# Performance work log

Hardware: AMD Instinct MI355X
Metric: run time of the kernel (lower is better)

## Reference

```python
import jax, jax.numpy as jnp
import numpy as np

MAX_DEG = 10
COUNTS = [10000, 250000, 300000, 250000, 120000, 40000, 15000, 8000, 4000, 2000, 1000]
STARTS = [int(s) for s in np.cumsum([0] + COUNTS[:-1])]
N_ATOMS = sum(COUNTS)  # 1,000,000
BATCH = 32768
N_TASKS, N_CLASSES = 12, 2
N_FEAT = 75
GC = [64, 64]
DENSE = 128
FD = 256
EPS = 1e-3  # keras BatchNormalization default epsilon


def _bn(x, gamma, beta, mean, var):
    # inference-mode batch norm (moving stats)
    return (x - mean) * jax.lax.rsqrt(var + EPS) * gamma + beta


def _graph_conv(atoms, deg_adjs, W, b):
    # W: [2*MAX_DEG+1, Cin, Cout]; order: (rel_d, self_d) for d=1..10, then self_0
    outs = [atoms[STARTS[0]:STARTS[0] + COUNTS[0]] @ W[2 * MAX_DEG] + b[2 * MAX_DEG]]
    for d in range(1, MAX_DEG + 1):
        rel = jnp.sum(atoms[deg_adjs[d - 1]], axis=1)          # [cnt_d, Cin]
        self_a = atoms[STARTS[d]:STARTS[d] + COUNTS[d]]        # [cnt_d, Cin]
        outs.append(rel @ W[2 * (d - 1)] + b[2 * (d - 1)] + self_a @ W[2 * d - 1] + b[2 * d - 1])
    return jax.nn.relu(jnp.concatenate(outs, axis=0))


def _graph_pool(atoms, deg_adjs):
    outs = [atoms[STARTS[0]:STARTS[0] + COUNTS[0]]]
    for d in range(1, MAX_DEG + 1):
        self_a = atoms[STARTS[d]:STARTS[d] + COUNTS[d]][:, None, :]  # [cnt_d,1,C]
        gathered = atoms[deg_adjs[d - 1]]                            # [cnt_d,d,C]
        outs.append(jnp.max(jnp.concatenate([self_a, gathered], axis=1), axis=1))
    return jnp.concatenate(outs, axis=0)


def setup_inputs() -> dict:
    key = jax.random.key(0)
    ks = jax.random.split(key, 48)
    inp = {}
    inp['atom_features'] = jax.random.normal(ks[0], (N_ATOMS, N_FEAT), jnp.float32)
    inp['degree_slice'] = jnp.asarray(np.stack([np.array(STARTS), np.array(COUNTS)], 1), jnp.int32)
    inp['membership'] = jax.random.randint(ks[1], (N_ATOMS,), 0, BATCH)
    inp['n_samples'] = BATCH
    for d in range(1, MAX_DEG + 1):
        inp[f'deg_adj_{d}'] = jax.random.randint(ks[1 + d], (COUNTS[d], d), 0, N_ATOMS)
    # GraphConv params: stacked [21, Cin, Cout]
    cin = N_FEAT
    for i, cout in enumerate(GC):
        inp[f'gc{i}_W'] = jax.random.normal(ks[12 + 2 * i], (2 * MAX_DEG + 1, cin, cout), jnp.float32) * 0.05
        inp[f'gc{i}_b'] = jnp.zeros((2 * MAX_DEG + 1, cout), jnp.float32)
        cin = cout
    # BatchNorm params (2 after graph convs: C=64; 1 after dense: C=128)
    for j, c in enumerate([GC[0], GC[1], DENSE]):
        inp[f'bn{j}_gamma'] = jnp.ones((c,), jnp.float32)
        inp[f'bn{j}_beta'] = jnp.zeros((c,), jnp.float32)
        inp[f'bn{j}_mean'] = jax.random.normal(ks[20 + j], (c,), jnp.float32) * 0.05
        inp[f'bn{j}_var'] = jax.random.uniform(ks[24 + j], (c,), jnp.float32, 0.5, 1.5)
    inp['dense_W'] = jax.random.normal(ks[30], (GC[-1], DENSE), jnp.float32) * 0.1
    inp['dense_b'] = jnp.zeros((DENSE,), jnp.float32)
    inp['fd0_W'] = jax.random.normal(ks[31], (2 * DENSE, FD), jnp.float32) * 0.06
    inp['fd0_b'] = jnp.zeros((FD,), jnp.float32)
    inp['rd_W'] = jax.random.normal(ks[32], (FD, N_TASKS * N_CLASSES), jnp.float32) * 0.06
    inp['rd_b'] = jnp.zeros((N_TASKS * N_CLASSES,), jnp.float32)
    return inp


def reference(atom_features, degree_slice, membership, n_samples,
              deg_adj_1, deg_adj_2, deg_adj_3, deg_adj_4, deg_adj_5,
              deg_adj_6, deg_adj_7, deg_adj_8, deg_adj_9, deg_adj_10,
              gc0_W, gc0_b, gc1_W, gc1_b,
              bn0_gamma, bn0_beta, bn0_mean, bn0_var,
              bn1_gamma, bn1_beta, bn1_mean, bn1_var,
              bn2_gamma, bn2_beta, bn2_mean, bn2_var,
              dense_W, dense_b, fd0_W, fd0_b, rd_W, rd_b):
    deg_adjs = [deg_adj_1, deg_adj_2, deg_adj_3, deg_adj_4, deg_adj_5,
                deg_adj_6, deg_adj_7, deg_adj_8, deg_adj_9, deg_adj_10]
    gc_W = [gc0_W, gc1_W]
    gc_b = [gc0_b, gc1_b]
    bns = [(bn0_gamma, bn0_beta, bn0_mean, bn0_var),
           (bn1_gamma, bn1_beta, bn1_mean, bn1_var)]
    x = atom_features
    for i in range(2):
        x = _graph_conv(x, deg_adjs, gc_W[i], gc_b[i])
        x = _bn(x, *bns[i])
        x = _graph_pool(x, deg_adjs)
    x = jax.nn.relu(x @ dense_W + dense_b)
    x = _bn(x, bn2_gamma, bn2_beta, bn2_mean, bn2_var)
    # GraphGather: per-molecule sum and max readout, then tanh
    s = jax.ops.segment_sum(x, membership, num_segments=BATCH)
    m = jax.ops.segment_max(x, membership, num_segments=BATCH)
    nf = jnp.tanh(jnp.concatenate([s, m], axis=1))  # [BATCH, 2*DENSE]
    h = jax.nn.relu(nf @ fd0_W + fd0_b)
    logits = (h @ rd_W + rd_b).reshape(BATCH, N_TASKS, N_CLASSES)
    logits = logits[:n_samples]  # TrimGraphOutput (static here)
    output = jax.nn.softmax(logits, axis=-1)
    return output, logits, nf
```

## Files before the change

### kernel.cpp

```cpp
#include <hip/hip_runtime.h>
#include <hip/hip_fp16.h>
#include <math.h>

namespace {

constexpr int NATOMS = 1000000;
constexpr int NBATCH = 32768;
constexpr int kCounts[11] = {10000,250000,300000,250000,120000,40000,15000,8000,4000,2000,1000};
constexpr int kStarts[11] = {0,10000,260000,560000,810000,930000,970000,985000,993000,997000,999000};
constexpr int X16S = 80;

struct AdjPtrs { const int* p[10]; };

typedef _Float16 h2 __attribute__((ext_vector_type(2)));
typedef _Float16 h8 __attribute__((ext_vector_type(8)));
typedef float    f4 __attribute__((ext_vector_type(4)));
union U32H2 { unsigned u; h2 h; };

__device__ __forceinline__ unsigned enc_f32(float x) {
    unsigned u = __float_as_uint(x);
    return (u & 0x80000000u) ? ~u : (u | 0x80000000u);
}
__device__ __forceinline__ float dec_f32(unsigned u) {
    return (u & 0x80000000u) ? __uint_as_float(u & 0x7FFFFFFFu) : __uint_as_float(~u);
}

__device__ __forceinline__ int swzS64d(int row, int k) { return row ^ (((k >> 2) & 7) << 2); }

__global__ __launch_bounds__(256) void cvt_kernel(const float* __restrict__ x,
                                                  __half* __restrict__ x16)
{
    const int row = blockIdx.x * 16 + (threadIdx.x >> 4);
    const int l16 = threadIdx.x & 15;
    if (row >= NATOMS) return;
    const float* __restrict__ xr = x + (size_t)row * 75;
    __half* __restrict__ xo = x16 + (size_t)row * X16S;
    #pragma unroll
    for (int q = 0; q < 5; ++q) {
        const int c = l16 + 16 * q;
        xo[c] = __float2half((c < 75) ? xr[c] : 0.f);
    }
}

__global__ __launch_bounds__(256) void packB_kernel(const float* __restrict__ W,
                                                    uint4* __restrict__ bp,
                                                    int CI, int GH, int KS)
{
    const int total = 11 * 4 * KS * 64;
    const int idx = blockIdx.x * 256 + threadIdx.x;
    if (idx >= total) return;
    const int lane = idx & 63;
    int q = idx >> 6;
    const int ks = q % KS; q /= KS;
    const int ni = q & 3;
    const int deg = q >> 2;
    const int col = ni * 16 + (lane & 15);
    __half vals[8];
    #pragma unroll
    for (int j = 0; j < 8; ++j) {
        const int k = ks * 32 + (lane >> 4) * 8 + j;
        float v = 0.f;
        if (k < GH * 8) {
            if (k < CI) {
                const int m = (deg == 0) ? 20 : (2 * deg - 1);
                v = W[((size_t)m * CI + k) * 64 + col];
            }
        } else {
            const int kk = k - GH * 8;
            if (deg > 0 && kk < CI)
                v = W[((size_t)(2 * (deg - 1)) * CI + kk) * 64 + col];
        }
        vals[j] = __float2half(v);
    }
    bp[idx] = *reinterpret_cast<const uint4*>(vals);
}

__global__ __launch_bounds__(256) void packBd_kernel(const float* __restrict__ Wd,
                                                     uint4* __restrict__ bpd)
{
    const int idx = blockIdx.x * 256 + threadIdx.x;
    if (idx >= 8 * 2 * 64) return;
    const int lane = idx & 63;
    const int q = idx >> 6;
    const int ks = q & 1, ni = q >> 1;
    const int col = ni * 16 + (lane & 15);
    __half vals[8];
    #pragma unroll
    for (int j = 0; j < 8; ++j) {
        const int k = ks * 32 + (lane >> 4) * 8 + j;
        vals[j] = __float2half(Wd[(size_t)k * 128 + col]);
    }
    bpd[idx] = *reinterpret_cast<const uint4*>(vals);
}

template<int D, int STRH, int GH>
__device__ __forceinline__ void stage_rel64_m(const __half* __restrict__ xin,
                                              const int* __restrict__ ad,
                                              int j0, int row, int l8,
                                              __half* __restrict__ s_a)
{
    int idxs[D];
    #pragma unroll
    for (int n = 0; n < D; ++n) idxs[n] = ad[(size_t)(j0 + row) * D + n];
    float2 r[4];
    #pragma unroll
    for (int q = 0; q < 4; ++q) r[q] = make_float2(0.f, 0.f);
    for (int n = 0; n < D; ++n) {
        const uint4 f4v = *reinterpret_cast<const uint4*>(xin + (size_t)idxs[n] * 64 + l8 * 8);
        const __half2* hh = reinterpret_cast<const __half2*>(&f4v);
        #pragma unroll
        for (int q = 0; q < 4; ++q) {
            const float2 v = __half22float2(hh[q]);
            r[q].x += v.x; r[q].y += v.y;
        }
    }
    uint4 o;
    unsigned* ou = reinterpret_cast<unsigned*>(&o);
    #pragma unroll
    for (int q = 0; q < 4; ++q) {
        U32H2 u; u.h = h2{(_Float16)r[q].x, (_Float16)r[q].y};
        ou[q] = u.u;
    }
    *reinterpret_cast<uint4*>(&s_a[row * STRH + (GH + l8) * 8]) = o;
}

template<int STRH, int GH>
__device__ __forceinline__ void stage_rel64_rt_m(const __half* __restrict__ xin,
                                                 const int* __restrict__ ad, int d,
                                                 int j0, int row, int l8,
                                                 __half* __restrict__ s_a)
{
    int idxs[10];
    for (int n = 0; n < d; ++n) idxs[n] = ad[(size_t)(j0 + row) * d + n];
    float2 r[4];
    #pragma unroll
    for (int q = 0; q < 4; ++q) r[q] = make_float2(0.f, 0.f);
    for (int n = 0; n < d; ++n) {
        const uint4 f4v = *reinterpret_cast<const uint4*>(xin + (size_t)idxs[n] * 64 + l8 * 8);
        const __half2* hh = reinterpret_cast<const __half2*>(&f4v);
        #pragma unroll
        for (int q = 0; q < 4; ++q) {
            const float2 v = __half22float2(hh[q]);
            r[q].x += v.x; r[q].y += v.y;
        }
    }
    uint4 o;
    unsigned* ou = reinterpret_cast<unsigned*>(&o);
    #pragma unroll
    for (int q = 0; q < 4; ++q) {
        U32H2 u; u.h = h2{(_Float16)r[q].x, (_Float16)r[q].y};
        ou[q] = u.u;
    }
    *reinterpret_cast<uint4*>(&s_a[row * STRH + (GH + l8) * 8]) = o;
}

template<int D, int STRH, int GH>
__device__ __forceinline__ void stage_rel75_m(const __half* __restrict__ xin,
                                              const int* __restrict__ ad,
                                              int j0, int row, int l8,
                                              __half* __restrict__ s_a)
{
    int idxs[D];
    #pragma unroll
    for (int n = 0; n < D; ++n) idxs[n] = ad[(size_t)(j0 + row) * D + n];
    float2 r[4], r2[4];
    #pragma unroll
    for (int q = 0; q < 4; ++q) { r[q] = make_float2(0.f, 0.f); r2[q] = make_float2(0.f, 0.f); }
    for (int n = 0; n < D; ++n) {
        const __half* __restrict__ xr = xin + (size_t)idxs[n] * X16S;
        const uint4 f4v = *reinterpret_cast<const uint4*>(xr + l8 * 8);
        const __half2* hh = reinterpret_cast<const __half2*>(&f4v);
        #pragma unroll
        for (int q = 0; q < 4; ++q) {
            const float2 v = __half22float2(hh[q]);
            r[q].x += v.x; r[q].y += v.y;
        }
        if (l8 < 2) {
            const uint4 g4 = *reinterpret_cast<const uint4*>(xr + 64 + l8 * 8);
            const __half2* t2 = reinterpret_cast<const __half2*>(&g4);
            #pragma unroll
            for (int q = 0; q < 4; ++q) {
                const float2 v = __half22float2(t2[q]);
                r2[q].x += v.x; r2[q].y += v.y;
            }
        }
    }
    uint4 o;
    unsigned* ou = reinterpret_cast<unsigned*>(&o);
    #pragma unroll
    for (int q = 0; q < 4; ++q) {
        U32H2 u; u.h = h2{(_Float16)r[q].x, (_Float16)r[q].y};
        ou[q] = u.u;
    }
    *reinterpret_cast<uint4*>(&s_a[row * STRH + (GH + l8) * 8]) = o;
    if (l8 < 2) {
        uint4 o2;
        unsigned* ou2 = reinterpret_cast<unsigned*>(&o2);
        #pragma unroll
        for (int q = 0; q < 4; ++q) {
            U32H2 u; u.h = h2{(_Float16)r2[q].x, (_Float16)r2[q].y};
            ou2[q] = u.u;
        }
        *reinterpret_cast<uint4*>(&s_a[row * STRH + (GH + 8 + l8) * 8]) = o2;
    }
}

template<int STRH, int GH>
__device__ __forceinline__ void stage_rel75_rt_m(const __half* __restrict__ xin,
                                                 const int* __restrict__ ad, int d,
                                                 int j0, int row, int l8,
                                                 __half* __restrict__ s_a)
{
    int idxs[10];
    for (int n = 0; n < d; ++n) idxs[n] = ad[(size_t)(j0 + row) * d + n];
    float2 r[4], r2[4];
    #pragma unroll
    for (int q = 0; q < 4; ++q) { r[q] = make_float2(0.f, 0.f); r2[q] = make_float2(0.f, 0.f); }
    for (int n = 0; n < d; ++n) {
        const __half* __restrict__ xr = xin + (size_t)idxs[n] * X16S;
        const uint4 f4v = *reinterpret_cast<const uint4*>(xr + l8 * 8);
        const __half2* hh = reinterpret_cast<const __half2*>(&f4v);
        #pragma unroll
        for (int q = 0; q < 4; ++q) {
            const float2 v = __half22float2(hh[q]);
            r[q].x += v.x; r[q].y += v.y;
        }
        if (l8 < 2) {
            const uint4 g4 = *reinterpret_cast<const uint4*>(xr + 64 + l8 * 8);
            const __half2* t2 = reinterpret_cast<const __half2*>(&g4);
            #pragma unroll
            for (int q = 0; q < 4; ++q) {
                const float2 v = __half22float2(t2[q]);
                r2[q].x += v.x; r2[q].y += v.y;
            }
        }
    }
    uint4 o;
    unsigned* ou = reinterpret_cast<unsigned*>(&o);
    #pragma unroll
    for (int q = 0; q < 4; ++q) {
        U32H2 u; u.h = h2{(_Float16)r[q].x, (_Float16)r[q].y};
        ou[q] = u.u;
    }
    *reinterpret_cast<uint4*>(&s_a[row * STRH + (GH + l8) * 8]) = o;
    if (l8 < 2) {
        uint4 o2;
        unsigned* ou2 = reinterpret_cast<unsigned*>(&o2);
        #pragma unroll
        for (int q = 0; q < 4; ++q) {
            U32H2 u; u.h = h2{(_Float16)r2[q].x, (_Float16)r2[q].y};
            ou2[q] = u.u;
        }
        *reinterpret_cast<uint4*>(&s_a[row * STRH + (GH + 8 + l8) * 8]) = o2;
    }
}

template<int CI>
__global__ __launch_bounds__(512) void conv_all_kernel(
    const __half* __restrict__ xin, AdjPtrs adj,
    const uint4* __restrict__ bp, const float* __restrict__ B,
    const float* __restrict__ bng, const float* __restrict__ bnb,
    const float* __restrict__ bnm, const float* __restrict__ bnv,
    __half* __restrict__ out)
{
    constexpr int XS   = (CI == 64) ? 64 : X16S;
    constexpr int GH   = (CI == 64) ? 8 : 10;
    constexpr int KS   = GH / 2;
    constexpr int STRH = 16 * GH + 8;
    __shared__ __align__(16) __half s_a[64 * STRH];

    int d = 0, rem = blockIdx.x;
    for (;;) { const int nb = (kCounts[d] + 63) >> 6; if (rem < nb) break; rem -= nb; ++d; }
    const int j0 = rem << 6;
    const int nA = min(64, kCounts[d] - j0);
    const int a0 = kStarts[d] + j0;
    const int t = threadIdx.x;
    const int row = t >> 3, l8 = t & 7;

    if (row < nA) {
        const __half* __restrict__ xr = xin + (size_t)(a0 + row) * XS;
        *reinterpret_cast<uint4*>(&s_a[row * STRH + l8 * 8]) =
            *reinterpret_cast<const uint4*>(xr + l8 * 8);
        if (CI == 75 && l8 < 2)
            *reinterpret_cast<uint4*>(&s_a[row * STRH + 64 + l8 * 8]) =
                *reinterpret_cast<const uint4*>(xr + 64 + l8 * 8);
    }

    if (d > 0) {
        if (row < nA) {
            const int* __restrict__ adp = adj.p[d - 1];
            if constexpr (CI == 64) {
                switch (d) {
                case 1: stage_rel64_m<1, STRH, GH>(xin, adp, j0, row, l8, s_a); break;
                case 2: stage_rel64_m<2, STRH, GH>(xin, adp, j0, row, l8, s_a); break;
                case 3: stage_rel64_m<3, STRH, GH>(xin, adp, j0, row, l8, s_a); break;
                case 4: stage_rel64_m<4, STRH, GH>(xin, adp, j0, row, l8, s_a); break;
                default: stage_rel64_rt_m<STRH, GH>(xin, adp, d, j0, row, l8, s_a); break;
                }
            } else {
                switch (d) {
                case 1: stage_rel75_m<1, STRH, GH>(xin, adp, j0, row, l8, s_a); break;
                case 2: stage_rel75_m<2, STRH, GH>(xin, adp, j0, row, l8, s_a); break;
                case 3: stage_rel75_m<3, STRH, GH>(xin, adp, j0, row, l8, s_a); break;
                case 4: stage_rel75_m<4, STRH, GH>(xin, adp, j0, row, l8, s_a); break;
                default: stage_rel75_rt_m<STRH, GH>(xin, adp, d, j0, row, l8, s_a); break;
                }
            }
        }
    } else {
        const uint4 z4 = make_uint4(0u, 0u, 0u, 0u);
        *reinterpret_cast<uint4*>(&s_a[row * STRH + (GH + l8) * 8]) = z4;
        if (CI == 75 && l8 < 2)
            *reinterpret_cast<uint4*>(&s_a[row * STRH + (GH + 8 + l8) * 8]) = z4;
    }
    __syncthreads();

    const int lane = t & 63, w = t >> 6;
    const int lr = lane & 15, lg = lane >> 4;

    #pragma unroll
    for (int sb = 0; sb < 2; ++sb) {
        const int s = 2 * w + sb;
        const int mi = s >> 2, ni = s & 3;
        f4 acc = {0.f, 0.f, 0.f, 0.f};
        #pragma unroll
        for (int ks = 0; ks < KS; ++ks) {
            const h8 av = *reinterpret_cast<const h8*>(
                &s_a[(mi * 16 + lr) * STRH + (ks * 4 + lg) * 8]);
            uint4 braw = bp[((d * 4 + ni) * KS + ks) * 64 + lane];
            const h8 bv = *reinterpret_cast<const h8*>(&braw);
            acc = __builtin_amdgcn_mfma_f32_16x16x32_f16(av, bv, acc, 0, 0, 0);
        }
        const int ch = ni * 16 + lr;
        const float bias = (d == 0) ? B[20 * 64 + ch]
                                    : (B[(2 * (d - 1)) * 64 + ch] + B[(2 * d - 1) * 64 + ch]);
        const float scl = rsqrtf(bnv[ch] + 1e-3f) * bng[ch];
        const float sht = bnb[ch] - bnm[ch] * scl;
        #pragma unroll
        for (int r = 0; r < 4; ++r) {
            const int atom = mi * 16 + lg * 4 + r;
            if (atom < nA)
                out[(size_t)(a0 + atom) * 64 + ch] =
                    __float2half(fmaf(fmaxf(acc[r] + bias, 0.f), scl, sht));
        }
    }
}

template<int D>
__device__ __forceinline__ void pool_rows(const __half* __restrict__ z,
                                          const int* __restrict__ ad, int j, int g8,
                                          float2 mx[4])
{
    int idxs[D];
    #pragma unroll
    for (int n = 0; n < D; ++n) idxs[n] = ad[(size_t)j * D + n];
    for (int n = 0; n < D; ++n) {
        const float4 f4v = *reinterpret_cast<const float4*>(z + (size_t)idxs[n] * 64 + g8 * 8);
        const __half2* hh = reinterpret_cast<const __half2*>(&f4v);
        #pragma unroll
        for (int q = 0; q < 4; ++q) {
            const float2 v = __half22float2(hh[q]);
            mx[q].x = fmaxf(mx[q].x, v.x);
            mx[q].y = fmaxf(mx[q].y, v.y);
        }
    }
}

__device__ __forceinline__ void pool_rows_rt(const __half* __restrict__ z,
                                             const int* __restrict__ ad, int d, int j, int g8,
                                             float2 mx[4])
{
    int idxs[10];
    for (int n = 0; n < d; ++n) idxs[n] = ad[(size_t)j * d + n];
    for (int n = 0; n < d; ++n) {
        const float4 f4v = *reinterpret_cast<const float4*>(z + (size_t)idxs[n] * 64 + g8 * 8);
        const __half2* hh = reinterpret_cast<const __half2*>(&f4v);
        #pragma unroll
        for (int q = 0; q < 4; ++q) {
            const float2 v = __half22float2(hh[q]);
            mx[q].x = fmaxf(mx[q].x, v.x);
            mx[q].y = fmaxf(mx[q].y, v.y);
        }
    }
}

__global__ __launch_bounds__(256) void pool_all_kernel(
    const __half* __restrict__ z, AdjPtrs adj, __half* __restrict__ p)
{
    int d = 0, rem = blockIdx.x;
    for (;;) { const int nb = (kCounts[d] + 31) >> 5; if (rem < nb) break; rem -= nb; ++d; }
    const int t = threadIdx.x;
    const int j = rem * 32 + (t >> 3);
    if (j >= kCounts[d]) return;
    const int g8 = t & 7;
    const int a = kStarts[d] + j;

    const float4 s4 = *reinterpret_cast<const float4*>(z + (size_t)a * 64 + g8 * 8);
    const __half2* sh2 = reinterpret_cast<const __half2*>(&s4);
    float2 mx[4];
    #pragma unroll
    for (int q = 0; q < 4; ++q) mx[q] = __half22float2(sh2[q]);

    if (d > 0) {
        const int* __restrict__ ad = adj.p[d - 1];
        switch (d) {
        case 1:  pool_rows<1 >(z, ad, j, g8, mx); break;
        case 2:  pool_rows<2 >(z, ad, j, g8, mx); break;
        case 3:  pool_rows<3 >(z, ad, j, g8, mx); break;
        case 4:  pool_rows<4 >(z, ad, j, g8, mx); break;
        default: pool_rows_rt(z, ad, d, j, g8, mx); break;
        }
    }

    union { __half2 h[4]; float4 f; } u;
    #pragma unroll
    for (int q = 0; q < 4; ++q) u.h[q] = __floats2half2_rn(mx[q].x, mx[q].y);
    *reinterpret_cast<float4*>(p + (size_t)a * 64 + g8 * 8) = u.f;
}

__global__ __launch_bounds__(256) void hist_kernel(const int* __restrict__ mem,
                                                   int* __restrict__ cnt)
{
    const int a = blockIdx.x * 256 + threadIdx.x;
    if (a < NATOMS) atomicAdd(&cnt[mem[a]], 1);
}

__global__ __launch_bounds__(512) void scan_kernel(const int* __restrict__ cnt,
                                                   int* __restrict__ off,
                                                   int* __restrict__ cur)
{
    __shared__ int part[512];
    const int t = threadIdx.x;
    const int base = t * 64;
    int s = 0;
    #pragma unroll 8
    for (int i = 0; i < 64; ++i) s += cnt[base + i];
    part[t] = s;
    __syncthreads();
    for (int o = 1; o < 512; o <<= 1) {
        int v = (t >= o) ? part[t - o] : 0;
        __syncthreads();
        part[t] += v;
        __syncthreads();
    }
    int run = (t == 0) ? 0 : part[t - 1];
    for (int i = 0; i < 64; ++i) {
        off[base + i] = run;
        cur[base + i] = run;
        run += cnt[base + i];
    }
}

__global__ __launch_bounds__(256) void scatter_kernel(const int* __restrict__ mem,
                                                      int* __restrict__ cur,
                                                      int* __restrict__ sorted,
                                                      int* __restrict__ sid)
{
    const int a = blockIdx.x * 256 + threadIdx.x;
    if (a < NATOMS) {
        const int m = mem[a];
        const int pos = atomicAdd(&cur[m], 1);
        sorted[pos] = a;
        sid[pos] = m;
    }
}

__global__ void seg_init_kernel(float* __restrict__ segS, unsigned* __restrict__ segM)
{
    const int n = NBATCH * 128;
    for (int i = blockIdx.x * blockDim.x + threadIdx.x; i < n; i += gridDim.x * blockDim.x) {
        segS[i] = 0.f;
        segM[i] = 0x007FFFFFu;
    }
}

__global__ __launch_bounds__(256) void dense_seg_sorted_kernel(
    const __half* __restrict__ p,
    const int* __restrict__ sorted, const int* __restrict__ sid,
    const uint4* __restrict__ bpd, const float* __restrict__ bd,
    const float* __restrict__ bng, const float* __restrict__ bnb,
    const float* __restrict__ bnm, const float* __restrict__ bnv,
    float* __restrict__ segS, unsigned* __restrict__ segM)
{
    __shared__ __align__(16) __half s_a[64 * 72];
    __shared__ __align__(16) float vbuf[64 * 64];
    __shared__ int s_idx[64];
    __shared__ int s_sid[64];

    const int t = threadIdx.x;
    const int pos0 = blockIdx.x * 64;

    if (t < 64) {
        s_idx[t] = sorted[pos0 + t];
        s_sid[t] = sid[pos0 + t];
    }
    __syncthreads();

    {
        const int row = t >> 3, l8 = t & 7;
        #pragma unroll
        for (int half = 0; half < 2; ++half) {
            const int rr = row + half * 32;
            *reinterpret_cast<uint4*>(&s_a[rr * 72 + l8 * 8]) =
                *reinterpret_cast<const uint4*>(p + (size_t)s_idx[rr] * 64 + l8 * 8);
        }
    }
    __syncthreads();

    const int lane = t & 63, w = t >> 6;
    const int lr = lane & 15, lg = lane >> 4;

    h8 av[2];
    #pragma unroll
    for (int ks = 0; ks < 2; ++ks)
        av[ks] = *reinterpret_cast<const h8*>(&s_a[(w * 16 + lr) * 72 + (ks * 4 + lg) * 8]);

    f4 acc[8];
    #pragma unroll
    for (int ni = 0; ni < 8; ++ni) {
        acc[ni] = f4{0.f, 0.f, 0.f, 0.f};
        #pragma unroll
        for (int ks = 0; ks < 2; ++ks) {
            uint4 braw = bpd[(ni * 2 + ks) * 64 + lane];
            const h8 bv = *reinterpret_cast<const h8*>(&braw);
            acc[ni] = __builtin_amdgcn_mfma_f32_16x16x32_f16(av[ks], bv, acc[ni], 0, 0, 0);
        }
    }

    #pragma unroll
    for (int half = 0; half < 2; ++half) {
        #pragma unroll
        for (int q = 0; q < 4; ++q) {
            const int ni = half * 4 + q;
            const int ch = ni * 16 + lr;
            const float bias = bd[ch];
            const float scl = rsqrtf(bnv[ch] + 1e-3f) * bng[ch];
            const float sht = bnb[ch] - bnm[ch] * scl;
            #pragma unroll
            for (int r = 0; r < 4; ++r) {
                const int atom = w * 16 + lg * 4 + r;
                vbuf[atom * 64 + (ch & 63)] =
                    fmaf(fmaxf(acc[ni][r] + bias, 0.f), scl, sht);
            }
        }
        __syncthreads();

        const int c = t & 63;
        const int rbase = (t >> 6) * 16;
        const int gch = half * 64 + c;
        int cur = s_sid[rbase];
        float s = 0.f, mx = -INFINITY;
        for (int r = rbase; r < rbase + 16; ++r) {
            const int sd = s_sid[r];
            if (sd != cur) {
                atomicAdd(&segS[(size_t)cur * 128 + gch], s);
                atomicMax(&segM[(size_t)cur * 128 + gch], enc_f32(mx));
                cur = sd; s = 0.f; mx = -INFINITY;
            }
            const float v = vbuf[r * 64 + c];
            s += v;
            mx = fmaxf(mx, v);
        }
        atomicAdd(&segS[(size_t)cur * 128 + gch], s);
        atomicMax(&segM[(size_t)cur * 128 + gch], enc_f32(mx));
        __syncthreads();
    }
}

__global__ void nf_fin_kernel(const float* __restrict__ segS,
                              const unsigned* __restrict__ segM,
                              float* __restrict__ nf)
{
    const int i = blockIdx.x * blockDim.x + threadIdx.x;
    const int m = i >> 7, c = i & 127;
    nf[(size_t)m * 256 + c]       = tanhf(segS[i]);
    nf[(size_t)m * 256 + 128 + c] = tanhf(dec_f32(segM[i]));
}

__global__ __launch_bounds__(256) void fd0_kernel(
    const float* __restrict__ nf, const float* __restrict__ W, const float* __restrict__ b,
    float* __restrict__ h)
{
    __shared__ __align__(16) float sx[256][64];
    const int t = threadIdx.x;
    const int r0 = (blockIdx.x >> 2) * 64;
    const int c0 = (blockIdx.x & 3) * 64;
    for (int ch = 0; ch < 4; ++ch) {
        for (int v = t; v < 1024; v += 256) {
            const int row = v >> 4, k0 = (v & 15) * 4 + ch * 64;
            const float4 r = *reinterpret_cast<const float4*>(nf + (size_t)(r0 + row) * 256 + k0);
            sx[k0 + 0][swzS64d(row, k0 + 0)] = r.x;
            sx[k0 + 1][swzS64d(row, k0 + 1)] = r.y;
            sx[k0 + 2][swzS64d(row, k0 + 2)] = r.z;
            sx[k0 + 3][swzS64d(row, k0 + 3)] = r.w;
        }
    }
    __syncthreads();

    const int c4 = (t & 15) * 4;
    const int a4 = (t >> 4) * 4;

    float acc[4][4];
    #pragma unroll
    for (int i = 0; i < 4; ++i)
        #pragma unroll
        for (int j = 0; j < 4; ++j) acc[i][j] = 0.f;

    for (int k = 0; k < 256; ++k) {
        const int sw = ((k >> 2) & 7) << 2;
        const float4 sv = *reinterpret_cast<const float4*>(&sx[k][a4 ^ sw]);
        const float4 w = *reinterpret_cast<const float4*>(W + (size_t)k * 256 + c0 + c4);
        const float ss[4] = {sv.x, sv.y, sv.z, sv.w};
        #pragma unroll
        for (int i = 0; i < 4; ++i) {
            acc[i][0] = fmaf(ss[i], w.x, acc[i][0]);
            acc[i][1] = fmaf(ss[i], w.y, acc[i][1]);
            acc[i][2] = fmaf(ss[i], w.z, acc[i][2]);
            acc[i][3] = fmaf(ss[i], w.w, acc[i][3]);
        }
    }

    const float4 bb = *reinterpret_cast<const float4*>(b + c0 + c4);
    const float bi[4] = {bb.x, bb.y, bb.z, bb.w};
    #pragma unroll
    for (int i = 0; i < 4; ++i) {
        float4 o;
        o.x = fmaxf(acc[i][0] + bi[0], 0.f);
        o.y = fmaxf(acc[i][1] + bi[1], 0.f);
        o.z = fmaxf(acc[i][2] + bi[2], 0.f);
        o.w = fmaxf(acc[i][3] + bi[3], 0.f);
        *reinterpret_cast<float4*>(h + (size_t)(r0 + a4 + i) * 256 + c0 + c4) = o;
    }
}

__global__ __launch_bounds__(384) void rd_kernel(
    const float* __restrict__ h, const float* __restrict__ W, const float* __restrict__ b,
    float* __restrict__ outP, float* __restrict__ outL)
{
    __shared__ float sh[32][257];
    const int t = threadIdx.x;
    const int r0 = blockIdx.x * 32;
    for (int e = t; e < 32 * 256; e += 384) {
        const int ri = e >> 8, k = e & 255;
        sh[ri][k] = h[(size_t)(r0 + ri) * 256 + k];
    }
    __syncthreads();
    const int r = t / 12, pj = t % 12;
    float a0 = b[2 * pj], a1 = b[2 * pj + 1];
    for (int k = 0; k < 256; ++k) {
        const float hv = sh[r][k];
        a0 = fmaf(hv, W[k * 24 + 2 * pj],     a0);
        a1 = fmaf(hv, W[k * 24 + 2 * pj + 1], a1);
    }
    const size_t m = (size_t)(r0 + r);
    outL[m * 24 + 2 * pj]     = a0;
    outL[m * 24 + 2 * pj + 1] = a1;
    const float mx = fmaxf(a0, a1);
    const float e0 = expf(a0 - mx), e1 = expf(a1 - mx);
    const float inv = 1.f / (e0 + e1);
    outP[m * 24 + 2 * pj]     = e0 * inv;
    outP[m * 24 + 2 * pj + 1] = e1 * inv;
}

}

extern "C" void kernel_launch(void* const* d_in, const int* in_sizes, int n_in,
                              void* d_out, int out_size, void* d_ws, size_t ws_size,
                              hipStream_t stream)
{
    const float* x       = (const float*)d_in[0];
    const int*   mem     = (const int*)d_in[2];
    AdjPtrs adj;
    for (int d = 0; d < 10; ++d) adj.p[d] = (const int*)d_in[4 + d];
    const float* gc0_W = (const float*)d_in[14];
    const float* gc0_b = (const float*)d_in[15];
    const float* gc1_W = (const float*)d_in[16];
    const float* gc1_b = (const float*)d_in[17];
    const float* bn0g = (const float*)d_in[18], *bn0b = (const float*)d_in[19];
    const float* bn0m = (const float*)d_in[20], *bn0v = (const float*)d_in[21];
    const float* bn1g = (const float*)d_in[22], *bn1b = (const float*)d_in[23];
    const float* bn1m = (const float*)d_in[24], *bn1v = (const float*)d_in[25];
    const float* bn2g = (const float*)d_in[26], *bn2b = (const float*)d_in[27];
    const float* bn2m = (const float*)d_in[28], *bn2v = (const float*)d_in[29];
    const float* dW   = (const float*)d_in[30], *db   = (const float*)d_in[31];
    const float* fW   = (const float*)d_in[32], *fb   = (const float*)d_in[33];
    const float* rW   = (const float*)d_in[34], *rb   = (const float*)d_in[35];

    __half* z16 = (__half*)d_ws;
    __half* p16 = z16 + (size_t)NATOMS * 64;
    __half* x16 = p16 + (size_t)NATOMS * 64;
    float*  hbuf = (float*)(x16 + (size_t)NATOMS * X16S);
    float*  segS = hbuf + (size_t)NBATCH * 256;
    unsigned* segM = (unsigned*)(segS + (size_t)NBATCH * 128);
    int*    cnt    = (int*)(segM + (size_t)NBATCH * 128);
    int*    offp   = cnt + NBATCH;
    int*    cur    = offp + NBATCH;
    int*    sorted = cur + NBATCH;
    int*    sid    = sorted + NATOMS;
    uint4*  bp0    = (uint4*)(sid + NATOMS);
    uint4*  bp1    = bp0 + 11 * 4 * 5 * 64;
    uint4*  bpd    = bp1 + 11 * 4 * 4 * 64;

    float* outP = (float*)d_out;
    float* outL = outP + (size_t)NBATCH * 24;
    float* nfb  = outL + (size_t)NBATCH * 24;

    int convBlocks = 0, poolBlocks = 0;
    for (int d = 0; d <= 10; ++d) {
        convBlocks += (kCounts[d] + 63) >> 6;
        poolBlocks += (kCounts[d] + 31) >> 5;
    }

    cvt_kernel<<<(NATOMS + 15) / 16, 256, 0, stream>>>(x, x16);
    packB_kernel<<<55, 256, 0, stream>>>(gc0_W, bp0, 75, 10, 5);
    packB_kernel<<<44, 256, 0, stream>>>(gc1_W, bp1, 64, 8, 4);
    packBd_kernel<<<4, 256, 0, stream>>>(dW, bpd);

    hipMemsetAsync(cnt, 0, NBATCH * sizeof(int), stream);
    hist_kernel<<<(NATOMS + 255) / 256, 256, 0, stream>>>(mem, cnt);
    scan_kernel<<<1, 512, 0, stream>>>(cnt, offp, cur);
    scatter_kernel<<<(NATOMS + 255) / 256, 256, 0, stream>>>(mem, cur, sorted, sid);
    seg_init_kernel<<<2048, 256, 0, stream>>>(segS, segM);

    conv_all_kernel<75><<<convBlocks, 512, 0, stream>>>(x16, adj, bp0, gc0_b,
                                                        bn0g, bn0b, bn0m, bn0v, z16);
    pool_all_kernel<<<poolBlocks, 256, 0, stream>>>(z16, adj, p16);

    conv_all_kernel<64><<<convBlocks, 512, 0, stream>>>(p16, adj, bp1, gc1_b,
                                                        bn1g, bn1b, bn1m, bn1v, z16);
    pool_all_kernel<<<poolBlocks, 256, 0, stream>>>(z16, adj, p16);

    dense_seg_sorted_kernel<<<NATOMS / 64, 256, 0, stream>>>(
        p16, sorted, sid, bpd, db, bn2g, bn2b, bn2m, bn2v, segS, segM);
    nf_fin_kernel<<<(NBATCH * 128) / 256, 256, 0, stream>>>(segS, segM, nfb);
    fd0_kernel<<<(NBATCH / 64) * 4, 256, 0, stream>>>(nfb, fW, fb, hbuf);
    rd_kernel<<<NBATCH / 32, 384, 0, stream>>>(hbuf, rW, rb, outP, outL);
}
```

Baseline: 1.021 ms.

## Fuse tanh readout into fd0 and run fd0 GEMM on fp16 MFMA

Measured after the change: 979.7 us. 1.04x faster.

```diff
diff --git a/kernel.cpp b/kernel.cpp
--- a/kernel.cpp
+++ b/kernel.cpp
@@ -24,8 +24,6 @@
 __device__ __forceinline__ float dec_f32(unsigned u) {
     return (u & 0x80000000u) ? __uint_as_float(u & 0x7FFFFFFFu) : __uint_as_float(~u);
 }
-
-__device__ __forceinline__ int swzS64d(int row, int k) { return row ^ (((k >> 2) & 7) << 2); }
 
 __global__ __launch_bounds__(256) void cvt_kernel(const float* __restrict__ x,
                                                   __half* __restrict__ x16)
@@ -91,6 +89,24 @@
         vals[j] = __float2half(Wd[(size_t)k * 128 + col]);
     }
     bpd[idx] = *reinterpret_cast<const uint4*>(vals);
+}
+
+__global__ __launch_bounds__(256) void packBf_kernel(const float* __restrict__ Wf,
+                                                     uint4* __restrict__ bpf)
+{
+    const int idx = blockIdx.x * 256 + threadIdx.x;
+    if (idx >= 16 * 8 * 64) return;
+    const int lane = idx & 63;
+    const int q = idx >> 6;
+    const int ks = q & 7, ni = q >> 3;
+    const int col = ni * 16 + (lane & 15);
+    __half vals[8];
+    #pragma unroll
+    for (int j = 0; j < 8; ++j) {
+        const int k = ks * 32 + (lane >> 4) * 8 + j;
+        vals[j] = __float2half(Wf[(size_t)k * 256 + col]);
+    }
+    bpf[idx] = *reinterpret_cast<const uint4*>(vals);
 }
 
 template<int D, int STRH, int GH>
@@ -567,69 +583,65 @@
     }
 }
 
-__global__ void nf_fin_kernel(const float* __restrict__ segS,
-                              const unsigned* __restrict__ segM,
-                              float* __restrict__ nf)
-{
-    const int i = blockIdx.x * blockDim.x + threadIdx.x;
-    const int m = i >> 7, c = i & 127;
-    nf[(size_t)m * 256 + c]       = tanhf(segS[i]);
-    nf[(size_t)m * 256 + 128 + c] = tanhf(dec_f32(segM[i]));
-}
-
-__global__ __launch_bounds__(256) void fd0_kernel(
-    const float* __restrict__ nf, const float* __restrict__ W, const float* __restrict__ b,
-    float* __restrict__ h)
-{
-    __shared__ __align__(16) float sx[256][64];
+__global__ __launch_bounds__(256) void fd0_mfma_kernel(
+    const float* __restrict__ segS, const unsigned* __restrict__ segM,
+    const uint4* __restrict__ bpf, const float* __restrict__ fb,
+    float* __restrict__ nf, float* __restrict__ h)
+{
+    __shared__ __align__(16) __half s_a[64 * 264];
     const int t = threadIdx.x;
-    const int r0 = (blockIdx.x >> 2) * 64;
-    const int c0 = (blockIdx.x & 3) * 64;
-    for (int ch = 0; ch < 4; ++ch) {
-        for (int v = t; v < 1024; v += 256) {
-            const int row = v >> 4, k0 = (v & 15) * 4 + ch * 64;
-            const float4 r = *reinterpret_cast<const float4*>(nf + (size_t)(r0 + row) * 256 + k0);
-            sx[k0 + 0][swzS64d(row, k0 + 0)] = r.x;
-            sx[k0 + 1][swzS64d(row, k0 + 1)] = r.y;
-            sx[k0 + 2][swzS64d(row, k0 + 2)] = r.z;
-            sx[k0 + 3][swzS64d(row, k0 + 3)] = r.w;
+    const int m0 = blockIdx.x * 64;
+    const int lane = t & 63, w = t >> 6;
+
+    {
+        const int c4 = lane * 4;
+        #pragma unroll
+        for (int r = 0; r < 16; ++r) {
+            const int row = w * 16 + r;
+            const int m = m0 + row;
+            float v[4];
+            if (c4 < 128) {
+                const float4 sv = *reinterpret_cast<const float4*>(&segS[(size_t)m * 128 + c4]);
+                v[0] = tanhf(sv.x); v[1] = tanhf(sv.y); v[2] = tanhf(sv.z); v[3] = tanhf(sv.w);
+            } else {
+                const uint4 mv = *reinterpret_cast<const uint4*>(&segM[(size_t)m * 128 + c4 - 128]);
+                v[0] = tanhf(dec_f32(mv.x)); v[1] = tanhf(dec_f32(mv.y));
+                v[2] = tanhf(dec_f32(mv.z)); v[3] = tanhf(dec_f32(mv.w));
+            }
+            *reinterpret_cast<float4*>(&nf[(size_t)m * 256 + c4]) =
+                make_float4(v[0], v[1], v[2], v[3]);
+            __half hv[4];
+            #pragma unroll
+            for (int j = 0; j < 4; ++j) hv[j] = __float2half(v[j]);
+            *reinterpret_cast<uint2*>(&s_a[row * 264 + c4]) =
+                *reinterpret_cast<const uint2*>(hv);
         }
     }
     __syncthreads();
 
-    const int c4 = (t & 15) * 4;
-    const int a4 = (t >> 4) * 4;
-
-    float acc[4][4];
-    #pragma unroll
-    for (int i = 0; i < 4; ++i)
-        #pragma unroll
-        for (int j = 0; j < 4; ++j) acc[i][j] = 0.f;
-
-    for (int k = 0; k < 256; ++k) {
-        const int sw = ((k >> 2) & 7) << 2;
-        const float4 sv = *reinterpret_cast<const float4*>(&sx[k][a4 ^ sw]);
-        const float4 w = *reinterpret_cast<const float4*>(W + (size_t)k * 256 + c0 + c4);
-        const float ss[4] = {sv.x, sv.y, sv.z, sv.w};
-        #pragma unroll
-        for (int i = 0; i < 4; ++i) {
-            acc[i][0] = fmaf(ss[i], w.x, acc[i][0]);
-            acc[i][1] = fmaf(ss[i], w.y, acc[i][1]);
-            acc[i][2] = fmaf(ss[i], w.z, acc[i][2]);
-            acc[i][3] = fmaf(ss[i], w.w, acc[i][3]);
-        }
-    }
-
-    const float4 bb = *reinterpret_cast<const float4*>(b + c0 + c4);
-    const float bi[4] = {bb.x, bb.y, bb.z, bb.w};
-    #pragma unroll
-    for (int i = 0; i < 4; ++i) {
-        float4 o;
-        o.x = fmaxf(acc[i][0] + bi[0], 0.f);
-        o.y = fmaxf(acc[i][1] + bi[1], 0.f);
-        o.z = fmaxf(acc[i][2] + bi[2], 0.f);
-        o.w = fmaxf(acc[i][3] + bi[3], 0.f);
-        *reinterpret_cast<float4*>(h + (size_t)(r0 + a4 + i) * 256 + c0 + c4) = o;
+    const int lr = lane & 15, lg = lane >> 4;
+
+    h8 av[8];
+    #pragma unroll
+    for (int ks = 0; ks < 8; ++ks)
+        av[ks] = *reinterpret_cast<const h8*>(&s_a[(w * 16 + lr) * 264 + (ks * 4 + lg) * 8]);
+
+    #pragma unroll
+    for (int ni = 0; ni < 16; ++ni) {
+        f4 acc = {0.f, 0.f, 0.f, 0.f};
+        #pragma unroll
+        for (int ks = 0; ks < 8; ++ks) {
+            uint4 braw = bpf[(ni * 8 + ks) * 64 + lane];
+            const h8 bv = *reinterpret_cast<const h8*>(&braw);
+            acc = __builtin_amdgcn_mfma_f32_16x16x32_f16(av[ks], bv, acc, 0, 0, 0);
+        }
+        const int ch = ni * 16 + lr;
+        const float bb = fb[ch];
+        #pragma unroll
+        for (int r = 0; r < 4; ++r) {
+            const int row = w * 16 + lg * 4 + r;
+            h[(size_t)(m0 + row) * 256 + ch] = fmaxf(acc[r] + bb, 0.f);
+        }
     }
 }
 
@@ -700,6 +712,7 @@
     uint4*  bp0    = (uint4*)(sid + NATOMS);
     uint4*  bp1    = bp0 + 11 * 4 * 5 * 64;
     uint4*  bpd    = bp1 + 11 * 4 * 4 * 64;
+    uint4*  bpf    = bpd + 8 * 2 * 64;
 
     float* outP = (float*)d_out;
     float* outL = outP + (size_t)NBATCH * 24;
@@ -715,6 +728,7 @@
     packB_kernel<<<55, 256, 0, stream>>>(gc0_W, bp0, 75, 10, 5);
     packB_kernel<<<44, 256, 0, stream>>>(gc1_W, bp1, 64, 8, 4);
     packBd_kernel<<<4, 256, 0, stream>>>(dW, bpd);
+    packBf_kernel<<<32, 256, 0, stream>>>(fW, bpf);
 
     hipMemsetAsync(cnt, 0, NBATCH * sizeof(int), stream);
     hist_kernel<<<(NATOMS + 255) / 256, 256, 0, stream>>>(mem, cnt);
@@ -732,7 +746,6 @@
 
     dense_seg_sorted_kernel<<<NATOMS / 64, 256, 0, stream>>>(
         p16, sorted, sid, bpd, db, bn2g, bn2b, bn2m, bn2v, segS, segM);
-    nf_fin_kernel<<<(NBATCH * 128) / 256, 256, 0, stream>>>(segS, segM, nfb);
-    fd0_kernel<<<(NBATCH / 64) * 4, 256, 0, stream>>>(nfb, fW, fb, hbuf);
+    fd0_mfma_kernel<<<NBATCH / 64, 256, 0, stream>>>(segS, segM, bpf, fb, nfb, hbuf);
     rd_kernel<<<NBATCH / 32, 384, 0, stream>>>(hbuf, rW, rb, outP, outL);
 }
```
